# Performance work log

Measured on AMD Instinct MI355X. Metric: run time of the kernel, lower is better.

## Reference

```python
import jax, jax.numpy as jnp
import numpy as np

EPS = 1e-6
B, K, D = 512, 1024, 256  # batch, out_features, in_features


def setup_inputs() -> dict:
    key = jax.random.key(0)
    kx, kp, ka = jax.random.split(key, 3)
    x = jax.random.normal(kx, (B, D), dtype=jnp.float32)
    # project inputs inside the Poincare ball (norm < 1)
    x = 0.7 * x / (1.0 + jnp.linalg.norm(x, axis=-1, keepdims=True))
    # module inits p, a ~ U(-0.001, 0.001); tiny norms are already inside the ball
    p = jax.random.uniform(kp, (K, D), minval=-0.001, maxval=0.001, dtype=jnp.float32)
    a = jax.random.uniform(ka, (K, D), minval=-0.001, maxval=0.001, dtype=jnp.float32)
    return {"x": x, "p": p, "a": a}


def _mobius_add(u, v):
    # Mobius addition on the Poincare ball (c=1), broadcasting over leading dims
    u2 = jnp.sum(u * u, axis=-1, keepdims=True)
    v2 = jnp.sum(v * v, axis=-1, keepdims=True)
    uv = jnp.sum(u * v, axis=-1, keepdims=True)
    num = (1.0 + 2.0 * uv + v2) * u + (1.0 - u2) * v
    den = 1.0 + 2.0 * uv + u2 * v2
    return num / (den + EPS)


def reference(x, p, a):
    # x: [B, D]; p, a: [K, D]
    p2 = jnp.sum(p * p, axis=-1, keepdims=True)           # [K, 1]
    # parallel transport of a from origin to p: PT_{0->p}(a) = (1 - ||p||^2) a
    a_pt = (1.0 - p2) * a                                  # [K, D]
    lam_p = 2.0 / (1.0 - p2 + EPS)                         # [K, 1] conformal factor at p
    # broadcast hyperplane math instead of materializing .repeat() copies
    z = _mobius_add(-p[None, :, :], x[:, None, :])         # [B, K, D] = (-p) (+) x
    z2 = jnp.sum(z * z, axis=-1)                           # [B, K]
    za = jnp.einsum('bkd,kd->bk', z, a_pt)                 # [B, K]
    na = jnp.linalg.norm(a_pt, axis=-1)                    # [K]
    # Ganea hyperbolic MLR logit: lam_p * ||a|| * asinh(2<z,a> / ((1-||z||^2)||a||))
    logits = lam_p[:, 0][None, :] * na[None, :] * jnp.arcsinh(
        2.0 * za / ((1.0 - z2) * na[None, :] + EPS)
    )
    return logits  # [B, K]
```

## Files before the change

### kernel.cpp

```cpp
#include <hip/hip_runtime.h>
#include <math.h>

#define B_ 512
#define K_ 1024
#define D_ 256
#define EPS_ 1e-6f

#define BM 64
#define BN 32
#define BK 32
#define STR 40

using short8  = __attribute__((ext_vector_type(8))) short;
using floatx4 = __attribute__((ext_vector_type(4))) float;

__device__ __forceinline__ unsigned short f2bf(float f) {
    unsigned int u = __float_as_uint(f);
    u += 0x7FFFu + ((u >> 16) & 1u);
    return (unsigned short)(u >> 16);
}
__device__ __forceinline__ float bf2f(unsigned short h) {
    return __uint_as_float((unsigned int)h << 16);
}

__global__ __launch_bounds__(512) void hyp_mlr_mfma(
    const float* __restrict__ x,
    const float* __restrict__ p,
    const float* __restrict__ a,
    float* __restrict__ out)
{
    __shared__ __align__(16) unsigned short Xh[2][BM][STR];
    __shared__ __align__(16) unsigned short Xl[2][BM][STR];
    __shared__ __align__(16) unsigned short Ph[2][BN][STR];
    __shared__ __align__(16) unsigned short Pl[2][BN][STR];
    __shared__ __align__(16) unsigned short Ah[2][BN][STR];
    __shared__ __align__(16) unsigned short Al[2][BN][STR];
    __shared__ float  x2s[BM];
    __shared__ float4 scal[BN];

    const int t    = threadIdx.x;
    const int lane = t & 63;
    const int wave = t >> 6;
    const int k0   = blockIdx.x * BN;
    const int b0   = blockIdx.y * BM;

    const bool isx = (t < 256);
    int srow, scol;
    const float *gp0, *gp1;
    if (isx) {
        srow = t >> 2; scol = (t & 3) * 8;
        gp0 = x + (b0 + srow) * D_ + scol;
        gp1 = gp0 + 4;
    } else {
        const int q = t - 256;
        srow = q >> 3; scol = (q & 7) * 4;
        gp0 = p + (k0 + srow) * D_ + scol;
        gp1 = a + (k0 + srow) * D_ + scol;
    }

    float s0 = 0.f, s1 = 0.f, s2 = 0.f;

    auto cvt_store = [&](int buf, float4 v0, float4 v1) {
        if (isx) {
            float e[8] = {v0.x, v0.y, v0.z, v0.w, v1.x, v1.y, v1.z, v1.w};
            unsigned int hp[4], lp[4];
#pragma unroll
            for (int j = 0; j < 4; ++j) {
                const float e0 = e[2 * j], e1 = e[2 * j + 1];
                const unsigned short h0 = f2bf(e0), h1 = f2bf(e1);
                hp[j] = (unsigned int)h0 | ((unsigned int)h1 << 16);
                lp[j] = (unsigned int)f2bf(e0 - bf2f(h0))
                      | ((unsigned int)f2bf(e1 - bf2f(h1)) << 16);
                s0 = fmaf(e0, e0, fmaf(e1, e1, s0));
            }
            *(uint4*)&Xh[buf][srow][scol] = make_uint4(hp[0], hp[1], hp[2], hp[3]);
            *(uint4*)&Xl[buf][srow][scol] = make_uint4(lp[0], lp[1], lp[2], lp[3]);
        } else {
            float ep[4] = {v0.x, v0.y, v0.z, v0.w};
            float ea[4] = {v1.x, v1.y, v1.z, v1.w};
            unsigned int hp[2], lp[2], ha[2], la[2];
#pragma unroll
            for (int j = 0; j < 2; ++j) {
                const float pe0 = ep[2 * j], pe1 = ep[2 * j + 1];
                const float ae0 = ea[2 * j], ae1 = ea[2 * j + 1];
                const unsigned short hp0 = f2bf(pe0), hp1 = f2bf(pe1);
                const unsigned short ha0 = f2bf(ae0), ha1 = f2bf(ae1);
                hp[j] = (unsigned int)hp0 | ((unsigned int)hp1 << 16);
                lp[j] = (unsigned int)f2bf(pe0 - bf2f(hp0))
                      | ((unsigned int)f2bf(pe1 - bf2f(hp1)) << 16);
                ha[j] = (unsigned int)ha0 | ((unsigned int)ha1 << 16);
                la[j] = (unsigned int)f2bf(ae0 - bf2f(ha0))
                      | ((unsigned int)f2bf(ae1 - bf2f(ha1)) << 16);
                s0 = fmaf(pe0, pe0, fmaf(pe1, pe1, s0));
                s1 = fmaf(ae0, ae0, fmaf(ae1, ae1, s1));
                s2 = fmaf(pe0, ae0, fmaf(pe1, ae1, s2));
            }
            *(uint2*)&Ph[buf][srow][scol] = make_uint2(hp[0], hp[1]);
            *(uint2*)&Pl[buf][srow][scol] = make_uint2(lp[0], lp[1]);
            *(uint2*)&Ah[buf][srow][scol] = make_uint2(ha[0], ha[1]);
            *(uint2*)&Al[buf][srow][scol] = make_uint2(la[0], la[1]);
        }
    };

    const int wm = wave & 3, wn = wave >> 2;
    const int m0 = wm * 16, n0 = wn * 16;
    const int lr = lane & 15, lg = lane >> 4;

    floatx4 accD = {0.f, 0.f, 0.f, 0.f};
    floatx4 accA = {0.f, 0.f, 0.f, 0.f};

    cvt_store(0, *(const float4*)gp0, *(const float4*)gp1);
    __syncthreads();

    int buf = 0;
#pragma unroll
    for (int s = 0; s < D_ / BK; ++s) {
        float4 nv0, nv1;
        if (s < D_ / BK - 1) {
            nv0 = *(const float4*)(gp0 + (s + 1) * BK);
            nv1 = *(const float4*)(gp1 + (s + 1) * BK);
        }

        const short8 xh = *(const short8*)&Xh[buf][m0 + lr][lg * 8];
        const short8 xl = *(const short8*)&Xl[buf][m0 + lr][lg * 8];
        const short8 ph = *(const short8*)&Ph[buf][n0 + lr][lg * 8];
        const short8 pl = *(const short8*)&Pl[buf][n0 + lr][lg * 8];
        const short8 ah = *(const short8*)&Ah[buf][n0 + lr][lg * 8];
        const short8 al = *(const short8*)&Al[buf][n0 + lr][lg * 8];
        accD = __builtin_amdgcn_mfma_f32_16x16x32_bf16(xh, ph, accD, 0, 0, 0);
        accA = __builtin_amdgcn_mfma_f32_16x16x32_bf16(xh, ah, accA, 0, 0, 0);
        accD = __builtin_amdgcn_mfma_f32_16x16x32_bf16(xh, pl, accD, 0, 0, 0);
        accA = __builtin_amdgcn_mfma_f32_16x16x32_bf16(xh, al, accA, 0, 0, 0);
        accD = __builtin_amdgcn_mfma_f32_16x16x32_bf16(xl, ph, accD, 0, 0, 0);
        accA = __builtin_amdgcn_mfma_f32_16x16x32_bf16(xl, ah, accA, 0, 0, 0);

        if (s < D_ / BK - 1) cvt_store(buf ^ 1, nv0, nv1);
        __syncthreads();
        buf ^= 1;
    }

    if (isx) {
        s0 += __shfl_xor(s0, 1);
        s0 += __shfl_xor(s0, 2);
        if ((t & 3) == 0) x2s[srow] = s0;
    } else {
        s0 += __shfl_xor(s0, 1); s0 += __shfl_xor(s0, 2); s0 += __shfl_xor(s0, 4);
        s1 += __shfl_xor(s1, 1); s1 += __shfl_xor(s1, 2); s1 += __shfl_xor(s1, 4);
        s2 += __shfl_xor(s2, 1); s2 += __shfl_xor(s2, 2); s2 += __shfl_xor(s2, 4);
        if (((t - 256) & 7) == 0) {
            const float beta = 1.f - s0;
            scal[srow] = make_float4(s0, s2, beta * sqrtf(s1), beta);
        }
    }
    __syncthreads();

    const float4 sc  = scal[n0 + lr];
    const float  lam = 2.f / (sc.w + EPS_);
#pragma unroll
    for (int i = 0; i < 4; ++i) {
        const int   r    = m0 + lg * 4 + i;
        const float x2v  = x2s[r];
        const float dt   = accD[i];
        const float xa   = accA[i];
        const float alpha = 1.f + x2v - 2.f * dt;
        const float rg    = 1.f / (1.f - 2.f * dt + sc.x * x2v + EPS_);
        const float z2    = (alpha * alpha * sc.x - 2.f * alpha * sc.w * dt
                             + sc.w * sc.w * x2v) * rg * rg;
        const float za    = sc.w * (sc.w * xa - alpha * sc.y) * rg;
        const float arg   = 2.f * za / ((1.f - z2) * sc.z + EPS_);
        out[(b0 + r) * K_ + k0 + n0 + lr] = lam * sc.z * asinhf(arg);
    }
}

extern "C" void kernel_launch(void* const* d_in, const int* in_sizes, int n_in,
                              void* d_out, int out_size, void* d_ws, size_t ws_size,
                              hipStream_t stream) {
    const float* x = (const float*)d_in[0];
    const float* p = (const float*)d_in[1];
    const float* a = (const float*)d_in[2];
    float* out = (float*)d_out;

    dim3 grid(K_ / BN, B_ / BM);
    dim3 block(512);
    hyp_mlr_mfma<<<grid, block, 0, stream>>>(x, p, a, out);
}
```

Measured before the change: 68.11 us.

## Load full D slab into swizzled LDS once and drop p/a low-part MFMAs

Replaces the double-buffered 32-wide K-loop (with a barrier per step) with a single bulk load of all 256 columns of x, p and a into XOR-swizzled shared memory, followed by one barrier and an unrolled MFMA loop. The low-order bf16 split of p and a is removed, cutting MFMAs per step from 6 to 4 and halving p/a conversion work. This trades fewer syncs and less math for more LDS per block and no load/compute overlap, and it lowers precision on the p/a side. Norm partial sums are written to shared arrays and reduced in the epilogue instead of by shuffles.

```diff
diff --git a/kernel.cpp b/kernel.cpp
--- a/kernel.cpp
+++ b/kernel.cpp
@@ -8,18 +8,16 @@
 
 #define BM 64
 #define BN 32
-#define BK 32
-#define STR 40
 
 using short8  = __attribute__((ext_vector_type(8))) short;
 using floatx4 = __attribute__((ext_vector_type(4))) float;
 
-__device__ __forceinline__ unsigned short f2bf(float f) {
+static __device__ __forceinline__ unsigned short f2bf(float f) {
     unsigned int u = __float_as_uint(f);
     u += 0x7FFFu + ((u >> 16) & 1u);
     return (unsigned short)(u >> 16);
 }
-__device__ __forceinline__ float bf2f(unsigned short h) {
+static __device__ __forceinline__ float bf2f(unsigned short h) {
     return __uint_as_float((unsigned int)h << 16);
 }
 
@@ -29,40 +27,30 @@
     const float* __restrict__ a,
     float* __restrict__ out)
 {
-    __shared__ __align__(16) unsigned short Xh[2][BM][STR];
-    __shared__ __align__(16) unsigned short Xl[2][BM][STR];
-    __shared__ __align__(16) unsigned short Ph[2][BN][STR];
-    __shared__ __align__(16) unsigned short Pl[2][BN][STR];
-    __shared__ __align__(16) unsigned short Ah[2][BN][STR];
-    __shared__ __align__(16) unsigned short Al[2][BN][STR];
-    __shared__ float  x2s[BM];
-    __shared__ float4 scal[BN];
+    __shared__ __align__(16) unsigned short XhL[BM * 256];
+    __shared__ __align__(16) unsigned short XlL[BM * 256];
+    __shared__ __align__(16) unsigned short PL [BN * 256];
+    __shared__ __align__(16) unsigned short AL [BN * 256];
+    __shared__ __align__(16) float Sx [BM][4];
+    __shared__ __align__(16) float Sp [BN][8];
+    __shared__ __align__(16) float Sa [BN][8];
+    __shared__ __align__(16) float Spa[BN][8];
 
-    const int t    = threadIdx.x;
-    const int lane = t & 63;
-    const int wave = t >> 6;
-    const int k0   = blockIdx.x * BN;
-    const int b0   = blockIdx.y * BM;
+    const int t  = threadIdx.x;
+    const int k0 = blockIdx.x * BN;
+    const int b0 = blockIdx.y * BM;
 
-    const bool isx = (t < 256);
-    int srow, scol;
-    const float *gp0, *gp1;
-    if (isx) {
-        srow = t >> 2; scol = (t & 3) * 8;
-        gp0 = x + (b0 + srow) * D_ + scol;
-        gp1 = gp0 + 4;
-    } else {
-        const int q = t - 256;
-        srow = q >> 3; scol = (q & 7) * 4;
-        gp0 = p + (k0 + srow) * D_ + scol;
-        gp1 = a + (k0 + srow) * D_ + scol;
-    }
-
-    float s0 = 0.f, s1 = 0.f, s2 = 0.f;
-
-    auto cvt_store = [&](int buf, float4 v0, float4 v1) {
-        if (isx) {
-            float e[8] = {v0.x, v0.y, v0.z, v0.w, v1.x, v1.y, v1.z, v1.w};
+    if (t < 256) {
+        const int row = t & 63;
+        const int cq  = t >> 6;
+        const float* g = x + (b0 + row) * D_;
+        float s0 = 0.f;
+#pragma unroll
+        for (int i = 0; i < 8; ++i) {
+            const int c = cq + 4 * i;
+            const float4 v0 = *(const float4*)(g + c * 8);
+            const float4 v1 = *(const float4*)(g + c * 8 + 4);
+            const float e[8] = {v0.x, v0.y, v0.z, v0.w, v1.x, v1.y, v1.z, v1.w};
             unsigned int hp[4], lp[4];
 #pragma unroll
             for (int j = 0; j < 4; ++j) {
@@ -73,35 +61,51 @@
                       | ((unsigned int)f2bf(e1 - bf2f(h1)) << 16);
                 s0 = fmaf(e0, e0, fmaf(e1, e1, s0));
             }
-            *(uint4*)&Xh[buf][srow][scol] = make_uint4(hp[0], hp[1], hp[2], hp[3]);
-            *(uint4*)&Xl[buf][srow][scol] = make_uint4(lp[0], lp[1], lp[2], lp[3]);
-        } else {
-            float ep[4] = {v0.x, v0.y, v0.z, v0.w};
-            float ea[4] = {v1.x, v1.y, v1.z, v1.w};
-            unsigned int hp[2], lp[2], ha[2], la[2];
+            const int idx = row * 256 + ((c ^ (row & 7)) << 3);
+            *(uint4*)&XhL[idx] = make_uint4(hp[0], hp[1], hp[2], hp[3]);
+            *(uint4*)&XlL[idx] = make_uint4(lp[0], lp[1], lp[2], lp[3]);
+        }
+        Sx[row][cq] = s0;
+    } else {
+        const int q   = t - 256;
+        const int row = q & 31;
+        const int cq  = q >> 5;
+        const float* gp = p + (k0 + row) * D_;
+        const float* ga = a + (k0 + row) * D_;
+        float sp2 = 0.f, sa2 = 0.f, spa = 0.f;
 #pragma unroll
-            for (int j = 0; j < 2; ++j) {
+        for (int i = 0; i < 4; ++i) {
+            const int c = cq + 8 * i;
+            const float4 p0 = *(const float4*)(gp + c * 8);
+            const float4 p1 = *(const float4*)(gp + c * 8 + 4);
+            const float4 a0 = *(const float4*)(ga + c * 8);
+            const float4 a1 = *(const float4*)(ga + c * 8 + 4);
+            const float ep[8] = {p0.x, p0.y, p0.z, p0.w, p1.x, p1.y, p1.z, p1.w};
+            const float ea[8] = {a0.x, a0.y, a0.z, a0.w, a1.x, a1.y, a1.z, a1.w};
+            unsigned int wp[4], wa[4];
+#pragma unroll
+            for (int j = 0; j < 4; ++j) {
                 const float pe0 = ep[2 * j], pe1 = ep[2 * j + 1];
                 const float ae0 = ea[2 * j], ae1 = ea[2 * j + 1];
-                const unsigned short hp0 = f2bf(pe0), hp1 = f2bf(pe1);
-                const unsigned short ha0 = f2bf(ae0), ha1 = f2bf(ae1);
-                hp[j] = (unsigned int)hp0 | ((unsigned int)hp1 << 16);
-                lp[j] = (unsigned int)f2bf(pe0 - bf2f(hp0))
-                      | ((unsigned int)f2bf(pe1 - bf2f(hp1)) << 16);
-                ha[j] = (unsigned int)ha0 | ((unsigned int)ha1 << 16);
-                la[j] = (unsigned int)f2bf(ae0 - bf2f(ha0))
-                      | ((unsigned int)f2bf(ae1 - bf2f(ha1)) << 16);
-                s0 = fmaf(pe0, pe0, fmaf(pe1, pe1, s0));
-                s1 = fmaf(ae0, ae0, fmaf(ae1, ae1, s1));
-                s2 = fmaf(pe0, ae0, fmaf(pe1, ae1, s2));
+                wp[j] = (unsigned int)f2bf(pe0) | ((unsigned int)f2bf(pe1) << 16);
+                wa[j] = (unsigned int)f2bf(ae0) | ((unsigned int)f2bf(ae1) << 16);
+                sp2 = fmaf(pe0, pe0, fmaf(pe1, pe1, sp2));
+                sa2 = fmaf(ae0, ae0, fmaf(ae1, ae1, sa2));
+                spa = fmaf(pe0, ae0, fmaf(pe1, ae1, spa));
             }
-            *(uint2*)&Ph[buf][srow][scol] = make_uint2(hp[0], hp[1]);
-            *(uint2*)&Pl[buf][srow][scol] = make_uint2(lp[0], lp[1]);
-            *(uint2*)&Ah[buf][srow][scol] = make_uint2(ha[0], ha[1]);
-            *(uint2*)&Al[buf][srow][scol] = make_uint2(la[0], la[1]);
+            const int idx = row * 256 + ((c ^ (row & 7)) << 3);
+            *(uint4*)&PL[idx] = make_uint4(wp[0], wp[1], wp[2], wp[3]);
+            *(uint4*)&AL[idx] = make_uint4(wa[0], wa[1], wa[2], wa[3]);
         }
-    };
+        Sp [row][cq] = sp2;
+        Sa [row][cq] = sa2;
+        Spa[row][cq] = spa;
+    }
 
+    __syncthreads();
+
+    const int lane = t & 63;
+    const int wave = t >> 6;
     const int wm = wave & 3, wn = wave >> 2;
     const int m0 = wm * 16, n0 = wn * 16;
     const int lr = lane & 15, lg = lane >> 4;
@@ -109,66 +113,52 @@
     floatx4 accD = {0.f, 0.f, 0.f, 0.f};
     floatx4 accA = {0.f, 0.f, 0.f, 0.f};
 
-    cvt_store(0, *(const float4*)gp0, *(const float4*)gp1);
-    __syncthreads();
-
-    int buf = 0;
+    const int xbase = (m0 + lr) * 256;
+    const int pbase = (n0 + lr) * 256;
+    const int sw    = lr & 7;
 #pragma unroll
-    for (int s = 0; s < D_ / BK; ++s) {
-        float4 nv0, nv1;
-        if (s < D_ / BK - 1) {
-            nv0 = *(const float4*)(gp0 + (s + 1) * BK);
-            nv1 = *(const float4*)(gp1 + (s + 1) * BK);
-        }
-
-        const short8 xh = *(const short8*)&Xh[buf][m0 + lr][lg * 8];
-        const short8 xl = *(const short8*)&Xl[buf][m0 + lr][lg * 8];
-        const short8 ph = *(const short8*)&Ph[buf][n0 + lr][lg * 8];
-        const short8 pl = *(const short8*)&Pl[buf][n0 + lr][lg * 8];
-        const short8 ah = *(const short8*)&Ah[buf][n0 + lr][lg * 8];
-        const short8 al = *(const short8*)&Al[buf][n0 + lr][lg * 8];
-        accD = __builtin_amdgcn_mfma_f32_16x16x32_bf16(xh, ph, accD, 0, 0, 0);
-        accA = __builtin_amdgcn_mfma_f32_16x16x32_bf16(xh, ah, accA, 0, 0, 0);
-        accD = __builtin_amdgcn_mfma_f32_16x16x32_bf16(xh, pl, accD, 0, 0, 0);
-        accA = __builtin_amdgcn_mfma_f32_16x16x32_bf16(xh, al, accA, 0, 0, 0);
-        accD = __builtin_amdgcn_mfma_f32_16x16x32_bf16(xl, ph, accD, 0, 0, 0);
-        accA = __builtin_amdgcn_mfma_f32_16x16x32_bf16(xl, ah, accA, 0, 0, 0);
-
-        if (s < D_ / BK - 1) cvt_store(buf ^ 1, nv0, nv1);
-        __syncthreads();
-        buf ^= 1;
+    for (int ks = 0; ks < 8; ++ks) {
+        const int off = ((ks * 4 + lg) ^ sw) << 3;
+        const short8 xh = *(const short8*)&XhL[xbase + off];
+        const short8 xl = *(const short8*)&XlL[xbase + off];
+        const short8 pv = *(const short8*)&PL [pbase + off];
+        const short8 av = *(const short8*)&AL [pbase + off];
+        accD = __builtin_amdgcn_mfma_f32_16x16x32_bf16(xh, pv, accD, 0, 0, 0);
+        accA = __builtin_amdgcn_mfma_f32_16x16x32_bf16(xh, av, accA, 0, 0, 0);
+        accD = __builtin_amdgcn_mfma_f32_16x16x32_bf16(xl, pv, accD, 0, 0, 0);
+        accA = __builtin_amdgcn_mfma_f32_16x16x32_bf16(xl, av, accA, 0, 0, 0);
     }
 
-    if (isx) {
-        s0 += __shfl_xor(s0, 1);
-        s0 += __shfl_xor(s0, 2);
-        if ((t & 3) == 0) x2s[srow] = s0;
-    } else {
-        s0 += __shfl_xor(s0, 1); s0 += __shfl_xor(s0, 2); s0 += __shfl_xor(s0, 4);
-        s1 += __shfl_xor(s1, 1); s1 += __shfl_xor(s1, 2); s1 += __shfl_xor(s1, 4);
-        s2 += __shfl_xor(s2, 1); s2 += __shfl_xor(s2, 2); s2 += __shfl_xor(s2, 4);
-        if (((t - 256) & 7) == 0) {
-            const float beta = 1.f - s0;
-            scal[srow] = make_float4(s0, s2, beta * sqrtf(s1), beta);
-        }
-    }
-    __syncthreads();
-
-    const float4 sc  = scal[n0 + lr];
-    const float  lam = 2.f / (sc.w + EPS_);
+    const int kc = n0 + lr;
+    const float4 sp0 = *(const float4*)&Sp [kc][0];
+    const float4 sp1 = *(const float4*)&Sp [kc][4];
+    const float4 sa0 = *(const float4*)&Sa [kc][0];
+    const float4 sa1 = *(const float4*)&Sa [kc][4];
+    const float4 sq0 = *(const float4*)&Spa[kc][0];
+    const float4 sq1 = *(const float4*)&Spa[kc][4];
+    const float p2 = (sp0.x + sp0.y) + (sp0.z + sp0.w)
+                   + (sp1.x + sp1.y) + (sp1.z + sp1.w);
+    const float a2 = (sa0.x + sa0.y) + (sa0.z + sa0.w)
+                   + (sa1.x + sa1.y) + (sa1.z + sa1.w);
+    const float pa = (sq0.x + sq0.y) + (sq0.z + sq0.w)
+                   + (sq1.x + sq1.y) + (sq1.z + sq1.w);
+    const float beta = 1.f - p2;
+    const float na   = beta * sqrtf(a2);
+    const float lam  = 2.f / (beta + EPS_);
 #pragma unroll
     for (int i = 0; i < 4; ++i) {
-        const int   r    = m0 + lg * 4 + i;
-        const float x2v  = x2s[r];
-        const float dt   = accD[i];
-        const float xa   = accA[i];
+        const int r = m0 + lg * 4 + i;
+        const float4 sx = *(const float4*)&Sx[r][0];
+        const float x2v = (sx.x + sx.y) + (sx.z + sx.w);
+        const float dt  = accD[i];
+        const float xa  = accA[i];
         const float alpha = 1.f + x2v - 2.f * dt;
-        const float rg    = 1.f / (1.f - 2.f * dt + sc.x * x2v + EPS_);
-        const float z2    = (alpha * alpha * sc.x - 2.f * alpha * sc.w * dt
-                             + sc.w * sc.w * x2v) * rg * rg;
-        const float za    = sc.w * (sc.w * xa - alpha * sc.y) * rg;
-        const float arg   = 2.f * za / ((1.f - z2) * sc.z + EPS_);
-        out[(b0 + r) * K_ + k0 + n0 + lr] = lam * sc.z * asinhf(arg);
+        const float rg    = 1.f / (1.f - 2.f * dt + p2 * x2v + EPS_);
+        const float z2    = (alpha * alpha * p2 - 2.f * alpha * beta * dt
+                             + beta * beta * x2v) * rg * rg;
+        const float za    = beta * (beta * xa - alpha * pa) * rg;
+        const float arg   = 2.f * za / ((1.f - z2) * na + EPS_);
+        out[(b0 + r) * K_ + k0 + kc] = lam * na * asinhf(arg);
     }
 }
 
```

New measurement: 66.12 us. -2.9%, faster.
